# Performance work log

Hardware: AMD Instinct MI355X
Metric: run time of the kernel (lower is better)

Reference implementation:

```python
import jax, jax.numpy as jnp
import numpy as np

V, E, H, S, B = 32000, 256, 256, 128, 64
HID = 30  # DENSE_MLP_HIDDEN_SIZE


def setup_inputs() -> dict:
    key = jax.random.key(0)
    ks = jax.random.split(key, 12)
    concepts = jax.random.randint(ks[0], (S, B), 0, V)
    concepts_lengths = jax.random.randint(ks[1], (B,), 1, S + 1).at[0].set(S)
    sE = 1.0 / np.sqrt(E)
    sH = 1.0 / np.sqrt(H)
    s2H = 1.0 / np.sqrt(2 * H)
    sHID = 1.0 / np.sqrt(HID)
    return {
        "concepts": concepts,
        "concepts_lengths": concepts_lengths,
        "embedding": jax.random.normal(ks[2], (V, E), jnp.float32) * 0.02,
        "Wih_f": jax.random.normal(ks[3], (4 * H, E), jnp.float32) * sE,
        "Whh_f": jax.random.normal(ks[4], (4 * H, H), jnp.float32) * sH,
        "b_f": jax.random.normal(ks[5], (4 * H,), jnp.float32) * sH,
        "Wih_b": jax.random.normal(ks[6], (4 * H, E), jnp.float32) * sE,
        "Whh_b": jax.random.normal(ks[7], (4 * H, H), jnp.float32) * sH,
        "b_b": jax.random.normal(ks[8], (4 * H,), jnp.float32) * sH,
        "Ua": jax.random.normal(ks[9], (HID, 2 * H), jnp.float32) * s2H,
        "Wa": jax.random.normal(ks[10], (HID, 2 * H), jnp.float32) * s2H,
        "va": jax.random.normal(ks[11], (1, HID), jnp.float32) * sHID,
    }


def _lstm(x, Wih, Whh, b):
    # x: (S, B, E) -> outputs (S, B, H). PyTorch gate order: i, f, g, o.
    Bsz = x.shape[1]
    Hd = Whh.shape[1]
    h0 = jnp.zeros((Bsz, Hd), x.dtype)
    c0 = jnp.zeros((Bsz, Hd), x.dtype)

    def step(carry, xt):
        h, c = carry
        gates = xt @ Wih.T + h @ Whh.T + b
        i, f, g, o = jnp.split(gates, 4, axis=-1)
        c = jax.nn.sigmoid(f) * c + jax.nn.sigmoid(i) * jnp.tanh(g)
        h = jax.nn.sigmoid(o) * jnp.tanh(c)
        return (h, c), h

    _, hs = jax.lax.scan(step, (h0, c0), x)
    return hs


def _encode(concepts, concepts_lengths, embedding, Wih_f, Whh_f, b_f, Wih_b, Whh_b, b_b):
    emb = embedding[concepts]  # (S, B, E)
    t = jnp.arange(S)[:, None]  # (S, 1)
    lens = concepts_lengths[None, :]  # (1, B)
    valid = t < lens  # (S, B)
    # reverse each sequence within its valid length (packed biLSTM semantics)
    rev_idx = jnp.where(valid, lens - 1 - t, t)  # (S, B)
    fwd = _lstm(emb, Wih_f, Whh_f, b_f)
    x_rev = jnp.take_along_axis(emb, rev_idx[:, :, None], axis=0)
    bwd_rev = _lstm(x_rev, Wih_b, Whh_b, b_b)
    bwd = jnp.take_along_axis(bwd_rev, rev_idx[:, :, None], axis=0)
    h = jnp.concatenate([fwd, bwd], axis=-1) * valid[:, :, None]  # zero padding like pad_packed
    return h.transpose(1, 0, 2)  # (B, S, 2H)


def _edge_scores(enc, Ua, Wa, va):
    # scores[b, i, j] = va @ tanh(Ua @ enc[b,i] + Wa @ enc[b,j])
    u = enc @ Ua.T  # (B, S, HID) parent term
    w = enc @ Wa.T  # (B, S, HID) child term
    return jnp.tanh(u[:, :, None, :] + w[:, None, :, :]) @ va[0]  # (B, S, S)


def reference(concepts, concepts_lengths, embedding, Wih_f, Whh_f, b_f,
              Wih_b, Whh_b, b_b, Ua, Wa, va):
    enc = _encode(concepts, concepts_lengths, embedding,
                  Wih_f, Whh_f, b_f, Wih_b, Whh_b, b_b)
    scores = _edge_scores(enc, Ua, Wa, va)
    predictions = jnp.where(jax.nn.sigmoid(scores) >= 0.5, 1, 0)
    return scores, predictions
```

## Files before the change

### kernel.cpp

```cpp
#include <hip/hip_runtime.h>

#define V_  32000
#define E_  256
#define H_  256
#define S_  128
#define B_  64
#define HID_ 30

typedef float f32x2 __attribute__((ext_vector_type(2)));

__device__ __forceinline__ float sigmoid_acc(float x) {
    return 1.0f / (1.0f + expf(-x));
}
__device__ __forceinline__ float tanh_acc(float x) {
    return tanhf(x);
}
__device__ __forceinline__ float fast_tanh(float x) {
    return 1.f - 2.f * __builtin_amdgcn_rcpf(1.f + __expf(2.f * x));
}

__device__ __forceinline__ void store_l2x2(unsigned long long* p,
                                           unsigned long long a,
                                           unsigned long long b) {
    asm volatile("global_store_dwordx2 %2, %0, off\n\t"
                 "global_store_dwordx2 %2, %1, off offset:8"
                 :: "v"(a), "v"(b), "v"(p) : "memory");
}
__device__ __forceinline__ void load_l2x2(const unsigned long long* p,
                                          unsigned long long& a,
                                          unsigned long long& b) {
    asm volatile("global_load_dwordx2 %0, %2, off sc0\n\t"
                 "global_load_dwordx2 %1, %2, off offset:8 sc0\n\t"
                 "s_waitcnt vmcnt(0)"
                 : "=&v"(a), "=&v"(b) : "v"(p) : "memory");
}

__global__ __launch_bounds__(256) void prep_stream_kernel(
    const float* __restrict__ Whh_f, const float* __restrict__ Whh_b,
    float4* __restrict__ sT) {
    int i = blockIdx.x * 256 + threadIdx.x;
    if (i >= 12 * 1024) return;
    int r = i & 1023;
    int q = i >> 10;
    int j = q % 3;
    int side = (q % 6) / 3;
    int dir = q / 6;
    const float* Whh = dir ? Whh_b : Whh_f;
    const float* src = Whh + (size_t)r * H_ + side * 128 + 116 + 4 * j;
    sT[(size_t)q * 1024 + r] = make_float4(src[0], src[1], src[2], src[3]);
}

#define GKC 32
#define GLD 132

__global__ __launch_bounds__(256, 4) void gemm2_kernel(
    const int* __restrict__ concepts, const float* __restrict__ embedding,
    const float* __restrict__ Wih_f, const float* __restrict__ Wih_b,
    float* __restrict__ Xg) {
    __shared__ float As[GKC][GLD];
    __shared__ float Bs[GKC][GLD];
    const int dir = blockIdx.y;
    const float* Wih = dir ? Wih_b : Wih_f;
    const int mt = blockIdx.x >> 3;
    const int nt = blockIdx.x & 7;
    const int m0 = mt * 128, n0 = nt * 128;
    const int t = threadIdx.x;
    const int tm = (t & 15) * 4;
    const int tn = (t >> 4) * 4;

    int cid[4], rr[4];
#pragma unroll
    for (int i = 0; i < 4; ++i) {
        int flat = t + 256 * i;
        rr[i] = flat >> 3;
        cid[i] = concepts[m0 + rr[i]];
    }

    float acc[8][8];
#pragma unroll
    for (int i = 0; i < 8; ++i)
#pragma unroll
        for (int j = 0; j < 8; ++j) acc[i][j] = 0.f;

    for (int kk = 0; kk < E_; kk += GKC) {
        __syncthreads();
#pragma unroll
        for (int i = 0; i < 4; ++i) {
            int flat = t + 256 * i;
            int r = rr[i];
            int kq = (flat & 7) * 4;
            float4 av = *(const float4*)&embedding[(size_t)cid[i] * E_ + kk + kq];
            float4 bv = *(const float4*)&Wih[(size_t)(n0 + r) * E_ + kk + kq];
            As[kq + 0][r] = av.x; As[kq + 1][r] = av.y;
            As[kq + 2][r] = av.z; As[kq + 3][r] = av.w;
            Bs[kq + 0][r] = bv.x; Bs[kq + 1][r] = bv.y;
            Bs[kq + 2][r] = bv.z; Bs[kq + 3][r] = bv.w;
        }
        __syncthreads();
#pragma unroll
        for (int k = 0; k < GKC; ++k) {
            float4 a0 = *(const float4*)&As[k][tm];
            float4 a1 = *(const float4*)&As[k][tm + 64];
            float4 b0 = *(const float4*)&Bs[k][tn];
            float4 b1 = *(const float4*)&Bs[k][tn + 64];
            float am[8] = {a0.x, a0.y, a0.z, a0.w, a1.x, a1.y, a1.z, a1.w};
            float bn[8] = {b0.x, b0.y, b0.z, b0.w, b1.x, b1.y, b1.z, b1.w};
#pragma unroll
            for (int i = 0; i < 8; ++i)
#pragma unroll
                for (int j = 0; j < 8; ++j)
                    acc[i][j] = fmaf(am[i], bn[j], acc[i][j]);
        }
    }
    float* out = Xg + ((size_t)dir * 8192 + m0) * 1024 + n0;
#pragma unroll
    for (int i = 0; i < 8; ++i) {
        int mr = (i < 4) ? (tm + i) : (tm + 60 + i);
        *(float4*)&out[(size_t)mr * 1024 + tn] =
            make_float4(acc[i][0], acc[i][1], acc[i][2], acc[i][3]);
        *(float4*)&out[(size_t)mr * 1024 + tn + 64] =
            make_float4(acc[i][4], acc[i][5], acc[i][6], acc[i][7]);
    }
}

#define RP_ 39
#define LP_ 19

__global__ __launch_bounds__(512, 2) void lstm_ks3_kernel(
    const float* __restrict__ Xg,
    const float* __restrict__ Whh_f, const float* __restrict__ Whh_b,
    const float* __restrict__ b_f, const float* __restrict__ b_b,
    const int* __restrict__ lens,
    float* __restrict__ enc,
    unsigned long long* __restrict__ Fch,
    unsigned long long* __restrict__ Sch,
    const float4* __restrict__ sT) {
    extern __shared__ f32x2 Wl[];
    __shared__ f32x2 h_sh2[64];
    __shared__ float g_sh[2][128];
    const int w = blockIdx.x;
    const int side = w >> 7;
    const int P = w & 127;
    const int dir = P & 1, b = P >> 1;
    const int t = threadIdx.x;
    const int r0 = t, r1 = t + 512;
    const int ul = t & 127;
    const int gc = t >> 8;
    const bool mine = (((t >> 7) & 1) == side);
    const int base = side << 7;
    const int idx = (gc << 7) + ul;
    const float* Whh = dir ? Whh_b : Whh_f;
    const int len = lens[b];

    f32x2 w0[RP_], w1[RP_];
    {
        const f32x2* p0 = (const f32x2*)(Whh + (size_t)r0 * H_ + base);
        const f32x2* p1 = (const f32x2*)(Whh + (size_t)r1 * H_ + base);
#pragma unroll
        for (int j = 0; j < RP_; ++j) { w0[j] = p0[j]; w1[j] = p1[j]; }
#pragma unroll
        for (int j = 0; j < LP_; ++j) {
            Wl[j * 1024 + r0] = p0[RP_ + j];
            Wl[j * 1024 + r1] = p1[RP_ + j];
        }
    }
    const float* bias = dir ? b_b : b_f;
    const float bias0 = bias[r0], bias1 = bias[r1];
    const float4* sT0 = sT + (size_t)(dir * 6 + side * 3) * 1024;

    unsigned long long* fw0 = Fch + (((size_t)P * 2 + 0) * 2 + side) * 512 + 2 * idx;
    unsigned long long* fw1 = Fch + (((size_t)P * 2 + 1) * 2 + side) * 512 + 2 * idx;
    const unsigned long long* fr0 =
        Fch + (((size_t)P * 2 + 0) * 2 + (side ^ 1)) * 512 + 2 * idx;
    const unsigned long long* fr1 =
        Fch + (((size_t)P * 2 + 1) * 2 + (side ^ 1)) * 512 + 2 * idx;
    unsigned long long* sw0 = Sch + (((size_t)P * 2 + 0) * 2 + side) * 512 + 2 * idx;
    unsigned long long* sw1 = Sch + (((size_t)P * 2 + 1) * 2 + side) * 512 + 2 * idx;
    const unsigned long long* sr0 =
        Sch + (((size_t)P * 2 + 0) * 2 + (side ^ 1)) * 512 + 2 * idx;
    const unsigned long long* sr1 =
        Sch + (((size_t)P * 2 + 1) * 2 + (side ^ 1)) * 512 + 2 * idx;

    if (t < 64) h_sh2[t] = (f32x2){0.f, 0.f};
    float c = 0.f;
    __syncthreads();

    int srow = dir ? (len - 1) : 0;
    float x0 = 0.f, x1 = 0.f;
    if (mine) {
        const float* xp = Xg + ((size_t)dir * 8192 + (size_t)srow * B_ + b) * 1024;
        x0 = xp[r0]; x1 = xp[r1];
    }

    for (int s = 0; s < S_; ++s) {
        float4 s00 = sT0[r0], s01 = sT0[1024 + r0], s02 = sT0[2048 + r0];
        float4 s10 = sT0[r1], s11 = sT0[1024 + r1], s12 = sT0[2048 + r1];
        int srow_n = 0;
        float x0n = 0.f, x1n = 0.f;
        if (s + 1 < S_) {
            int ns = s + 1;
            srow_n = dir ? ((ns < len) ? (len - 1 - ns) : ns) : ns;
            if (mine) {
                const float* xp =
                    Xg + ((size_t)dir * 8192 + (size_t)srow_n * B_ + b) * 1024;
                x0n = xp[r0]; x1n = xp[r1];
            }
        }

        f32x2 a0 = (f32x2){0.f, 0.f}, a1 = (f32x2){0.f, 0.f};
#pragma unroll
        for (int j = 0; j < RP_; ++j) {
            f32x2 hv = h_sh2[j];
            a0 = __builtin_elementwise_fma(w0[j], hv, a0);
            a1 = __builtin_elementwise_fma(w1[j], hv, a1);
        }
#pragma unroll
        for (int j = 0; j < LP_; ++j) {
            f32x2 hv = h_sh2[RP_ + j];
            f32x2 wa = Wl[j * 1024 + r0];
            f32x2 wb = Wl[j * 1024 + r1];
            a0 = __builtin_elementwise_fma(wa, hv, a0);
            a1 = __builtin_elementwise_fma(wb, hv, a1);
        }
        {
            f32x2 h58 = h_sh2[58], h59 = h_sh2[59], h60 = h_sh2[60];
            f32x2 h61 = h_sh2[61], h62 = h_sh2[62], h63 = h_sh2[63];
            a0 = __builtin_elementwise_fma((f32x2){s00.x, s00.y}, h58, a0);
            a0 = __builtin_elementwise_fma((f32x2){s00.z, s00.w}, h59, a0);
            a0 = __builtin_elementwise_fma((f32x2){s01.x, s01.y}, h60, a0);
            a0 = __builtin_elementwise_fma((f32x2){s01.z, s01.w}, h61, a0);
            a0 = __builtin_elementwise_fma((f32x2){s02.x, s02.y}, h62, a0);
            a0 = __builtin_elementwise_fma((f32x2){s02.z, s02.w}, h63, a0);
            a1 = __builtin_elementwise_fma((f32x2){s10.x, s10.y}, h58, a1);
            a1 = __builtin_elementwise_fma((f32x2){s10.z, s10.w}, h59, a1);
            a1 = __builtin_elementwise_fma((f32x2){s11.x, s11.y}, h60, a1);
            a1 = __builtin_elementwise_fma((f32x2){s11.z, s11.w}, h61, a1);
            a1 = __builtin_elementwise_fma((f32x2){s12.x, s12.y}, h62, a1);
            a1 = __builtin_elementwise_fma((f32x2){s12.z, s12.w}, h63, a1);
        }
        float p0 = a0.x + a0.y, p1 = a1.x + a1.y;

        const unsigned tag = (unsigned)(s + 1);
        float iv = 0.f, gv = 0.f;
        if (!mine) {
            unsigned long long k0 =
                ((unsigned long long)tag << 32) | (unsigned long long)__float_as_uint(p0);
            unsigned long long k1 =
                ((unsigned long long)tag << 32) | (unsigned long long)__float_as_uint(p1);
            store_l2x2((s & 1) ? fw1 : fw0, k0, k1);
            unsigned long long* sb = (s & 1) ? sw1 : sw0;
            __hip_atomic_store(sb, k0, __ATOMIC_RELAXED, __HIP_MEMORY_SCOPE_AGENT);
            __hip_atomic_store(sb + 1, k1, __ATOMIC_RELAXED, __HIP_MEMORY_SCOPE_AGENT);
        } else {
            const unsigned long long* fr = (s & 1) ? fr1 : fr0;
            const unsigned long long* sr = (s & 1) ? sr1 : sr0;
            float q0f, q1f;
            for (;;) {
                unsigned long long f0, f1;
                load_l2x2(fr, f0, f1);
                if ((unsigned)(f0 >> 32) == tag && (unsigned)(f1 >> 32) == tag) {
                    q0f = __uint_as_float((unsigned)f0);
                    q1f = __uint_as_float((unsigned)f1);
                    break;
                }
                unsigned long long a0q = __hip_atomic_load(
                    sr, __ATOMIC_RELAXED, __HIP_MEMORY_SCOPE_AGENT);
                unsigned long long a1q = __hip_atomic_load(
                    sr + 1, __ATOMIC_RELAXED, __HIP_MEMORY_SCOPE_AGENT);
                if ((unsigned)(a0q >> 32) == tag && (unsigned)(a1q >> 32) == tag) {
                    q0f = __uint_as_float((unsigned)a0q);
                    q1f = __uint_as_float((unsigned)a1q);
                    break;
                }
            }
            float g0 = p0 + q0f + bias0 + x0;
            float g1 = p1 + q1f + bias1 + x1;
            if (gc == 0) {
                iv = sigmoid_acc(g0);
                gv = tanh_acc(g1);
            } else {
                g_sh[0][ul] = sigmoid_acc(g0);
                g_sh[1][ul] = sigmoid_acc(g1);
            }
        }
        __syncthreads();

        if (mine && gc == 0) {
            float fv = g_sh[0][ul], ov = g_sh[1][ul];
            c = fv * c + iv * gv;
            float h = ov * tanh_acc(c);
            ((float*)h_sh2)[ul] = h;
            int orow = dir ? srow : s;
            enc[((size_t)b * S_ + orow) * 512 + dir * H_ + base + ul] =
                (orow < len) ? h : 0.f;
        }
        __syncthreads();

        srow = srow_n;
        x0 = x0n; x1 = x1n;
    }
}

__global__ __launch_bounds__(256) void uw_kernel(
    const float* __restrict__ enc, const float* __restrict__ Ua,
    const float* __restrict__ Wa, float* __restrict__ U, float* __restrict__ Wout) {
    __shared__ float wgt[60][129];
    __shared__ float erow[4][128];
    const int tid = threadIdx.x;
    const int b = blockIdx.y, s0 = blockIdx.x * 32;
    const int rl = tid >> 6;
    const int d = tid & 63;
    const int dd = d & 31;
    const int isW = d >> 5;
    float acc[8];
#pragma unroll
    for (int i = 0; i < 8; ++i) acc[i] = 0.f;

    for (int kk = 0; kk < 4; ++kk) {
        __syncthreads();
        for (int i = tid; i < 30 * 128; i += 256) {
            int r = i >> 7, k = i & 127;
            wgt[r][k] = Ua[(size_t)r * 512 + kk * 128 + k];
            wgt[r + 30][k] = Wa[(size_t)r * 512 + kk * 128 + k];
        }
        for (int chunk = 0; chunk < 8; ++chunk) {
            __syncthreads();
            for (int i = tid; i < 4 * 128; i += 256) {
                int r = i >> 7, k = i & 127;
                erow[r][k] = enc[((size_t)b * S_ + (s0 + chunk * 4 + r)) * 512 + kk * 128 + k];
            }
            __syncthreads();
            if (dd < HID_) {
                const float* wr = wgt[dd + 30 * isW];
                const float* er = erow[rl];
                float a = acc[chunk];
#pragma unroll
                for (int k = 0; k < 128; ++k) a = fmaf(er[k], wr[k], a);
                acc[chunk] = a;
            }
        }
    }
    if (dd < HID_) {
        float* dst = isW ? Wout : U;
#pragma unroll
        for (int chunk = 0; chunk < 8; ++chunk)
            dst[((size_t)b * S_ + (s0 + chunk * 4 + rl)) * 32 + dd] = acc[chunk];
    }
}

__global__ __launch_bounds__(256) void scores_kernel(
    const float* __restrict__ U, const float* __restrict__ W,
    const float* __restrict__ va,
    float* __restrict__ scores, float* __restrict__ preds) {
    __shared__ float w_sh[128][31];
    const int b = blockIdx.y, i0 = blockIdx.x * 32;
    const int tid = threadIdx.x;

    float va_r[HID_];
#pragma unroll
    for (int d2 = 0; d2 < HID_; ++d2) va_r[d2] = va[d2];

    for (int i = tid; i < 128 * HID_; i += 256) {
        int r = i / HID_, d2 = i - r * HID_;
        w_sh[r][d2] = W[((size_t)b * S_ + r) * 32 + d2];
    }
    __syncthreads();

    const int il = tid >> 3;
    const int jb = (tid & 7) * 16;
    float u_r[HID_];
    const float* urow = U + ((size_t)b * S_ + i0 + il) * 32;
#pragma unroll
    for (int d2 = 0; d2 < HID_; ++d2) u_r[d2] = urow[d2];

    const size_t obase = ((size_t)b * S_ + (i0 + il)) * S_;
    for (int jj = 0; jj < 16; ++jj) {
        int j = jb + jj;
        float acc = 0.f;
#pragma unroll
        for (int d2 = 0; d2 < HID_; ++d2)
            acc = fmaf(va_r[d2], fast_tanh(u_r[d2] + w_sh[j][d2]), acc);
        scores[obase + j] = acc;
        preds[obase + j] = (sigmoid_acc(acc) >= 0.5f) ? 1.f : 0.f;
    }
}

extern "C" void kernel_launch(void* const* d_in, const int* in_sizes, int n_in,
                              void* d_out, int out_size, void* d_ws, size_t ws_size,
                              hipStream_t stream) {
    (void)in_sizes; (void)n_in; (void)out_size; (void)ws_size;
    const int* concepts = (const int*)d_in[0];
    const int* lens = (const int*)d_in[1];
    const float* embedding = (const float*)d_in[2];
    const float* Wih_f = (const float*)d_in[3];
    const float* Whh_f = (const float*)d_in[4];
    const float* b_f = (const float*)d_in[5];
    const float* Wih_b = (const float*)d_in[6];
    const float* Whh_b = (const float*)d_in[7];
    const float* b_b = (const float*)d_in[8];
    const float* Ua = (const float*)d_in[9];
    const float* Wa = (const float*)d_in[10];
    const float* va = (const float*)d_in[11];

    char* ws = (char*)d_ws;
    float* Xg = (float*)(ws + 0);
    float* enc = (float*)(ws + 67108864);
    float* U = (float*)(ws + 83886080);
    float* W = (float*)(ws + 84934656);
    unsigned long long* Fch = (unsigned long long*)(ws + 85983232);
    unsigned long long* Sch = (unsigned long long*)(ws + 88080384);
    float4* sT = (float4*)(ws + 90177536);

    float* scores = (float*)d_out;
    float* preds = scores + (size_t)B_ * S_ * S_;

    (void)hipMemsetAsync(Fch, 0, 2 * 2097152, stream);

    hipLaunchKernelGGL(prep_stream_kernel, dim3(48), dim3(256), 0, stream,
                       Whh_f, Whh_b, sT);
    hipLaunchKernelGGL(gemm2_kernel, dim3(512, 2), dim3(256), 0, stream,
                       concepts, embedding, Wih_f, Wih_b, Xg);

    {
        const float* XgA = Xg;
        void* ka[] = {(void*)&XgA, (void*)&Whh_f, (void*)&Whh_b, (void*)&b_f,
                      (void*)&b_b, (void*)&lens, (void*)&enc, (void*)&Fch,
                      (void*)&Sch, (void*)&sT};
        (void)hipLaunchCooperativeKernel((const void*)lstm_ks3_kernel, dim3(256),
                                         dim3(512), ka, LP_ * 1024 * sizeof(f32x2),
                                         stream);
    }

    hipLaunchKernelGGL(uw_kernel, dim3(4, 64), dim3(256), 0, stream,
                       enc, Ua, Wa, U, W);
    hipLaunchKernelGGL(scores_kernel, dim3(4, 64), dim3(256), 0, stream,
                       U, W, va, scores, preds);
}
```

Measured before the change: 602.4 us.

## Remap LSTM gate rows per wave to use shuffles and one barrier per step

Reassigns hidden-state rows so that each wave holds all four gates (i,g in the low half, f,o in the high half) for 32 hidden units. The gate combine then goes through __shfl_xor instead of a shared-memory exchange. The h buffer is double-buffered, which cuts the two __syncthreads per timestep to a single lightweight LDS barrier. It also raises the priority of producer waves, delays the fallback atomic poll behind a spin count, and replaces tanhf with a sigmoid-based tanh, with a slight numerical difference.

```diff
diff --git a/kernel.cpp b/kernel.cpp
--- a/kernel.cpp
+++ b/kernel.cpp
@@ -12,8 +12,8 @@
 __device__ __forceinline__ float sigmoid_acc(float x) {
     return 1.0f / (1.0f + expf(-x));
 }
-__device__ __forceinline__ float tanh_acc(float x) {
-    return tanhf(x);
+__device__ __forceinline__ float tanh_sig(float x) {
+    return 2.0f * sigmoid_acc(2.0f * x) - 1.0f;
 }
 __device__ __forceinline__ float fast_tanh(float x) {
     return 1.f - 2.f * __builtin_amdgcn_rcpf(1.f + __expf(2.f * x));
@@ -33,6 +33,12 @@
                  "global_load_dwordx2 %1, %2, off offset:8 sc0\n\t"
                  "s_waitcnt vmcnt(0)"
                  : "=&v"(a), "=&v"(b) : "v"(p) : "memory");
+}
+
+__device__ __forceinline__ void barrier_lds() {
+    asm volatile("s_waitcnt lgkmcnt(0)" ::: "memory");
+    __builtin_amdgcn_s_barrier();
+    __builtin_amdgcn_sched_barrier(0);
 }
 
 __global__ __launch_bounds__(256) void prep_stream_kernel(
@@ -125,6 +131,7 @@
 
 #define RP_ 39
 #define LP_ 19
+#define SPIN_FAST_ 10
 
 __global__ __launch_bounds__(512, 2) void lstm_ks3_kernel(
     const float* __restrict__ Xg,
@@ -136,36 +143,41 @@
     unsigned long long* __restrict__ Sch,
     const float4* __restrict__ sT) {
     extern __shared__ f32x2 Wl[];
-    __shared__ f32x2 h_sh2[64];
-    __shared__ float g_sh[2][128];
+    __shared__ f32x2 h_sh2[2][64];
     const int w = blockIdx.x;
     const int side = w >> 7;
     const int P = w & 127;
     const int dir = P & 1, b = P >> 1;
     const int t = threadIdx.x;
-    const int r0 = t, r1 = t + 512;
-    const int ul = t & 127;
-    const int gc = t >> 8;
-    const bool mine = (((t >> 7) & 1) == side);
+    const int wav = t >> 6;
+    const int lane = t & 63;
+    const int li = lane & 31;
+    const int half = lane >> 5;
+    const int qw = (wav & 1) | ((wav >> 2) << 1);
+    const bool mine = (((wav >> 1) & 1) == side);
+    const int hs = mine ? side : (side ^ 1);
+    const int hcol = (hs << 7) + (qw << 5) + li;
+    const int rA = hcol + half * 256;
+    const int rB = hcol + 512 + half * 256;
     const int base = side << 7;
-    const int idx = (gc << 7) + ul;
+    const int idx = (qw << 6) + lane;
     const float* Whh = dir ? Whh_b : Whh_f;
     const int len = lens[b];
 
     f32x2 w0[RP_], w1[RP_];
     {
-        const f32x2* p0 = (const f32x2*)(Whh + (size_t)r0 * H_ + base);
-        const f32x2* p1 = (const f32x2*)(Whh + (size_t)r1 * H_ + base);
+        const f32x2* p0 = (const f32x2*)(Whh + (size_t)rA * H_ + base);
+        const f32x2* p1 = (const f32x2*)(Whh + (size_t)rB * H_ + base);
 #pragma unroll
         for (int j = 0; j < RP_; ++j) { w0[j] = p0[j]; w1[j] = p1[j]; }
 #pragma unroll
         for (int j = 0; j < LP_; ++j) {
-            Wl[j * 1024 + r0] = p0[RP_ + j];
-            Wl[j * 1024 + r1] = p1[RP_ + j];
+            Wl[j * 1024 + t] = p0[RP_ + j];
+            Wl[j * 1024 + 512 + t] = p1[RP_ + j];
         }
     }
     const float* bias = dir ? b_b : b_f;
-    const float bias0 = bias[r0], bias1 = bias[r1];
+    const float bias0 = bias[rA], bias1 = bias[rB];
     const float4* sT0 = sT + (size_t)(dir * 6 + side * 3) * 1024;
 
     unsigned long long* fw0 = Fch + (((size_t)P * 2 + 0) * 2 + side) * 512 + 2 * idx;
@@ -181,7 +193,7 @@
     const unsigned long long* sr1 =
         Sch + (((size_t)P * 2 + 1) * 2 + (side ^ 1)) * 512 + 2 * idx;
 
-    if (t < 64) h_sh2[t] = (f32x2){0.f, 0.f};
+    if (t < 64) h_sh2[0][t] = (f32x2){0.f, 0.f};
     float c = 0.f;
     __syncthreads();
 
@@ -189,12 +201,13 @@
     float x0 = 0.f, x1 = 0.f;
     if (mine) {
         const float* xp = Xg + ((size_t)dir * 8192 + (size_t)srow * B_ + b) * 1024;
-        x0 = xp[r0]; x1 = xp[r1];
+        x0 = xp[rA]; x1 = xp[rB];
     }
 
     for (int s = 0; s < S_; ++s) {
-        float4 s00 = sT0[r0], s01 = sT0[1024 + r0], s02 = sT0[2048 + r0];
-        float4 s10 = sT0[r1], s11 = sT0[1024 + r1], s12 = sT0[2048 + r1];
+        if (!mine) __builtin_amdgcn_s_setprio(1);
+        float4 s00 = sT0[rA], s01 = sT0[1024 + rA], s02 = sT0[2048 + rA];
+        float4 s10 = sT0[rB], s11 = sT0[1024 + rB], s12 = sT0[2048 + rB];
         int srow_n = 0;
         float x0n = 0.f, x1n = 0.f;
         if (s + 1 < S_) {
@@ -203,28 +216,29 @@
             if (mine) {
                 const float* xp =
                     Xg + ((size_t)dir * 8192 + (size_t)srow_n * B_ + b) * 1024;
-                x0n = xp[r0]; x1n = xp[r1];
+                x0n = xp[rA]; x1n = xp[rB];
             }
         }
 
+        const f32x2* hb = h_sh2[s & 1];
         f32x2 a0 = (f32x2){0.f, 0.f}, a1 = (f32x2){0.f, 0.f};
 #pragma unroll
         for (int j = 0; j < RP_; ++j) {
-            f32x2 hv = h_sh2[j];
+            f32x2 hv = hb[j];
             a0 = __builtin_elementwise_fma(w0[j], hv, a0);
             a1 = __builtin_elementwise_fma(w1[j], hv, a1);
         }
 #pragma unroll
         for (int j = 0; j < LP_; ++j) {
-            f32x2 hv = h_sh2[RP_ + j];
-            f32x2 wa = Wl[j * 1024 + r0];
-            f32x2 wb = Wl[j * 1024 + r1];
+            f32x2 hv = hb[RP_ + j];
+            f32x2 wa = Wl[j * 1024 + t];
+            f32x2 wb = Wl[j * 1024 + 512 + t];
             a0 = __builtin_elementwise_fma(wa, hv, a0);
             a1 = __builtin_elementwise_fma(wb, hv, a1);
         }
         {
-            f32x2 h58 = h_sh2[58], h59 = h_sh2[59], h60 = h_sh2[60];
-            f32x2 h61 = h_sh2[61], h62 = h_sh2[62], h63 = h_sh2[63];
+            f32x2 h58 = hb[58], h59 = hb[59], h60 = hb[60];
+            f32x2 h61 = hb[61], h62 = hb[62], h63 = hb[63];
             a0 = __builtin_elementwise_fma((f32x2){s00.x, s00.y}, h58, a0);
             a0 = __builtin_elementwise_fma((f32x2){s00.z, s00.w}, h59, a0);
             a0 = __builtin_elementwise_fma((f32x2){s01.x, s01.y}, h60, a0);
@@ -241,7 +255,6 @@
         float p0 = a0.x + a0.y, p1 = a1.x + a1.y;
 
         const unsigned tag = (unsigned)(s + 1);
-        float iv = 0.f, gv = 0.f;
         if (!mine) {
             unsigned long long k0 =
                 ((unsigned long long)tag << 32) | (unsigned long long)__float_as_uint(p0);
@@ -251,10 +264,12 @@
             unsigned long long* sb = (s & 1) ? sw1 : sw0;
             __hip_atomic_store(sb, k0, __ATOMIC_RELAXED, __HIP_MEMORY_SCOPE_AGENT);
             __hip_atomic_store(sb + 1, k1, __ATOMIC_RELAXED, __HIP_MEMORY_SCOPE_AGENT);
+            __builtin_amdgcn_s_setprio(0);
         } else {
             const unsigned long long* fr = (s & 1) ? fr1 : fr0;
             const unsigned long long* sr = (s & 1) ? sr1 : sr0;
             float q0f, q1f;
+            int spin = 0;
             for (;;) {
                 unsigned long long f0, f1;
                 load_l2x2(fr, f0, f1);
@@ -263,38 +278,36 @@
                     q1f = __uint_as_float((unsigned)f1);
                     break;
                 }
-                unsigned long long a0q = __hip_atomic_load(
-                    sr, __ATOMIC_RELAXED, __HIP_MEMORY_SCOPE_AGENT);
-                unsigned long long a1q = __hip_atomic_load(
-                    sr + 1, __ATOMIC_RELAXED, __HIP_MEMORY_SCOPE_AGENT);
-                if ((unsigned)(a0q >> 32) == tag && (unsigned)(a1q >> 32) == tag) {
-                    q0f = __uint_as_float((unsigned)a0q);
-                    q1f = __uint_as_float((unsigned)a1q);
-                    break;
+                if (++spin > SPIN_FAST_) {
+                    unsigned long long a0q = __hip_atomic_load(
+                        sr, __ATOMIC_RELAXED, __HIP_MEMORY_SCOPE_AGENT);
+                    unsigned long long a1q = __hip_atomic_load(
+                        sr + 1, __ATOMIC_RELAXED, __HIP_MEMORY_SCOPE_AGENT);
+                    if ((unsigned)(a0q >> 32) == tag && (unsigned)(a1q >> 32) == tag) {
+                        q0f = __uint_as_float((unsigned)a0q);
+                        q1f = __uint_as_float((unsigned)a1q);
+                        break;
+                    }
                 }
             }
             float g0 = p0 + q0f + bias0 + x0;
             float g1 = p1 + q1f + bias1 + x1;
-            if (gc == 0) {
-                iv = sigmoid_acc(g0);
-                gv = tanh_acc(g1);
-            } else {
-                g_sh[0][ul] = sigmoid_acc(g0);
-                g_sh[1][ul] = sigmoid_acc(g1);
+            float e0 = sigmoid_acc(g0);
+            float u, v;
+            if (half == 0) { u = e0 * tanh_sig(g1); v = 0.f; }
+            else           { u = e0; v = sigmoid_acc(g1); }
+            float fx = __shfl_xor(u, 32);
+            float ox = __shfl_xor(v, 32);
+            if (half == 0) {
+                c = fx * c + u;
+                float h = ox * tanh_sig(c);
+                ((float*)h_sh2[(s + 1) & 1])[(qw << 5) + li] = h;
+                int orow = dir ? srow : s;
+                enc[((size_t)b * S_ + orow) * 512 + dir * H_ + base + (qw << 5) + li] =
+                    (orow < len) ? h : 0.f;
             }
         }
-        __syncthreads();
-
-        if (mine && gc == 0) {
-            float fv = g_sh[0][ul], ov = g_sh[1][ul];
-            c = fv * c + iv * gv;
-            float h = ov * tanh_acc(c);
-            ((float*)h_sh2)[ul] = h;
-            int orow = dir ? srow : s;
-            enc[((size_t)b * S_ + orow) * 512 + dir * H_ + base + ul] =
-                (orow < len) ? h : 0.f;
-        }
-        __syncthreads();
+        barrier_lds();
 
         srow = srow_n;
         x0 = x0n; x1 = x1n;
```

Result: slower. 695.0 us (+15.4%).
